# Performance work log

Measured on AMD Instinct MI355X. Metric: run time of the kernel, lower is better.

## Reference

```python
import jax, jax.numpy as jnp
import numpy as np

T, B, F_, H, D, C = 16, 1024, 512, 128, 8, 100  # trees, batch, feat, hidden, depth, classes
L = 2 ** (D + 1)  # n_leaf = 512


def _routing_tables():
    # Static per-leaf routing: node index and branch side at each depth.
    # Derived from compute_mu's gather indices:
    #   node(d, l) = 2^d - 1 + l // 2^(D+1-d);  side(d, l) = (l // 2^(D-d)) % 2
    l = np.arange(L)
    node = np.stack([(2 ** d - 1) + l // (2 ** (D + 1 - d)) for d in range(D + 1)])  # [D+1, L]
    side = np.stack([(l // (2 ** (D - d))) % 2 for d in range(D + 1)])               # [D+1, L]
    return jnp.asarray(node, dtype=jnp.int32), jnp.asarray(side.astype(np.bool_))


def setup_inputs() -> dict:
    key = jax.random.key(0)
    ks = jax.random.split(key, 4)
    return {
        "feat": jax.random.normal(ks[0], (B, F_), jnp.float32),
        "W1": jax.random.normal(ks[1], (T, F_, H), jnp.float32) * 0.05,
        "b1": jnp.zeros((T, H), jnp.float32),
        "W2": jax.random.normal(ks[2], (T, H, L), jnp.float32) * 0.05,
        "b2": jnp.zeros((T, L), jnp.float32),
        "pi": jax.random.uniform(ks[3], (T, L, C), jnp.float32, -2.0, 2.0),
    }


def reference(feat, W1, b1, W2, b2, pi):
    node, side = _routing_tables()
    # Per-tree MLP head (dropout is identity in eval mode).
    h = jax.nn.relu(jnp.einsum('bf,tfh->tbh', feat, W1) + b1[:, None, :])        # [T,B,H]
    p = jax.nn.sigmoid(jnp.einsum('tbh,thl->tbl', h, W2) + b2[:, None, :])       # [T,B,L]
    # compute_mu: product of routing probs along each root->leaf path.
    sel = p[:, :, node]                          # [T,B,D+1,L] gather (static indices)
    route = jnp.where(side, 1.0 - sel, sel)      # left -> p, right -> 1-p
    mu = jnp.prod(route, axis=2)                 # [T,B,L]
    # compute_py_x: mean over leaves then mean over trees of mu @ softmax(pi).
    leaf_p = jax.nn.softmax(pi, axis=-1)         # [T,L,C]
    py_x = jnp.einsum('tbl,tlc->bc', mu, leaf_p) / (L * T)  # [B,C]
    return jnp.log(py_x)
```

## Files before the change

### kernel.cpp

```cpp
#include <hip/hip_runtime.h>
#include <hip/hip_bf16.h>
#include <math.h>

#define T_ 16
#define B_ 1024
#define F_ 512
#define H_ 128
#define D_ 8
#define C_ 100
#define L_ 512
#define CP_ 112

typedef __attribute__((ext_vector_type(8))) short bf16x8_t;
typedef __attribute__((ext_vector_type(4))) float f32x4_t;

__device__ inline ushort f2bf(float x) {
  __hip_bfloat16 b = __float2bfloat16(x);
  return *(ushort*)&b;
}
__device__ inline float bf2f(ushort u) {
  union { unsigned int i; float f; } v;
  v.i = ((unsigned int)u) << 16;
  return v.f;
}

__device__ inline void bar_raw() {
  asm volatile("" ::: "memory");
  __builtin_amdgcn_s_barrier();
  asm volatile("" ::: "memory");
}
__device__ inline void bar_publish_lds() {
  asm volatile("s_waitcnt lgkmcnt(0)" ::: "memory");
  __builtin_amdgcn_s_barrier();
  asm volatile("" ::: "memory");
}

__global__ __launch_bounds__(256) void k_prep(
    const float* __restrict__ W1, const float* __restrict__ W2,
    const float* __restrict__ pi, ushort* __restrict__ W1T,
    ushort* __restrict__ W2T, ushort* __restrict__ lpT) {
  __shared__ float tile[64][68];
  ushort (*tileT)[48] = (ushort(*)[48])tile;
  const int bid = blockIdx.x, tid = threadIdx.x;

  if (bid < 512) {
    const float* X; ushort* XT; int K, N, kb, nb, s;
    if (bid < 256) {
      int u = bid & 15;  kb = u & 7;  nb = (u >> 3) & 1;  s = bid >> 4;
      X = W1; XT = W1T; K = F_; N = H_;
    } else {
      int r = bid - 256; int u = r & 15; kb = u & 1; nb = (u >> 1) & 7; s = r >> 4;
      X = W2; XT = W2T; K = H_; N = L_;
    }
    const int k0 = kb * 64, n0 = nb * 64;
    const float* Xs = X + (size_t)s * K * N;
    ushort* XTs = XT + (size_t)s * N * K;
    {
      const int rrow = tid >> 4, c4 = (tid & 15) * 4;
#pragma unroll
      for (int j = 0; j < 4; ++j) {
        float4 v = *(const float4*)(Xs + (size_t)(k0 + j * 16 + rrow) * N + n0 + c4);
        *(float4*)&tile[j * 16 + rrow][c4] = v;
      }
    }
    __syncthreads();
    {
      const int k8 = (tid & 7) * 8;
#pragma unroll
      for (int pass = 0; pass < 2; ++pass) {
        int rr = pass * 32 + (tid >> 3);
        bf16x8_t o;
#pragma unroll
        for (int i = 0; i < 8; ++i) o[i] = (short)f2bf(tile[k8 + i][rr]);
        *(bf16x8_t*)(XTs + (size_t)(n0 + rr) * K + k0 + k8) = o;
      }
    }
    return;
  }
  {
    int bid2 = bid - 512;
    int t = bid2 >> 4, l0 = (bid2 & 15) << 5;
    int lane = tid & 63;
#pragma unroll
    for (int p = 0; p < 8; ++p) {
      int rl = p * 4 + (tid >> 6);
      const float* x = pi + (size_t)(t * L_ + l0 + rl) * C_;
      float v0 = (lane < C_) ? x[lane] : -1e30f;
      float v1 = (lane + 64 < C_) ? x[lane + 64] : -1e30f;
      float m = fmaxf(v0, v1);
#pragma unroll
      for (int off = 32; off; off >>= 1) m = fmaxf(m, __shfl_xor(m, off, 64));
      float e0 = __expf(v0 - m);
      float e1 = (lane + 64 < C_) ? __expf(v1 - m) : 0.0f;
      float sm = e0 + e1;
#pragma unroll
      for (int off = 32; off; off >>= 1) sm += __shfl_xor(sm, off, 64);
      float inv = 1.0f / sm;
      if (lane < C_) tileT[lane][rl] = f2bf(e0 * inv);
      int c2 = lane + 64;
      if (c2 < CP_) tileT[c2][rl] = f2bf(c2 < C_ ? e1 * inv : 0.0f);
    }
    __syncthreads();
    ushort* dst = lpT + (size_t)t * CP_ * L_ + l0;
    for (int idx = tid; idx < 448; idx += 256) {
      int c = idx >> 2, ch = (idx & 3) * 8;
      *(bf16x8_t*)(dst + (size_t)c * L_ + ch) = *(const bf16x8_t*)&tileT[c][ch];
    }
  }
}

__global__ __launch_bounds__(512, 4) void k12_mfma(
    const float* __restrict__ feat, const ushort* __restrict__ W1T,
    const float* __restrict__ b1, const ushort* __restrict__ W2T,
    const float* __restrict__ b2, const ushort* __restrict__ lpT,
    float* __restrict__ part) {
  __shared__ ushort smem[38400];
  ushort (*h_s)[136] = (ushort(*)[136])smem;
  ushort (*a_s0)[72] = (ushort(*)[72])(smem + 4352);
  ushort (*a_s1)[72] = (ushort(*)[72])(smem + 4352 + 2304);
  ushort (*b_s0)[72] = (ushort(*)[72])(smem + 8960);
  ushort (*b_s1)[72] = (ushort(*)[72])(smem + 8960 + 9216);
  ushort (*w_s0)[136] = (ushort(*)[136])(smem + 4352);
  ushort (*w_s1)[136] = (ushort(*)[136])(smem + 4352 + 8704);
  ushort (*p_s)[520] = (ushort(*)[520])(smem + 21760);

  const int bid = blockIdx.x;
  const int t = bid & 15, b0 = (bid >> 4) * 32;
  const int tid = threadIdx.x;
  const int w = tid >> 6, lane = tid & 63, quad = lane >> 4, n = lane & 15;

  {
    const bool doA = tid < 256;
    const int srow = tid >> 3, scol = (tid & 7) * 8;
    const float*  fp32p = feat + (size_t)(b0 + srow) * F_ + scol;
    const ushort* w1p   = W1T + ((size_t)t * H_ + srow) * F_ + scol;

    float4 ra[2][2];
    bf16x8_t rb[2][2];

    if (doA) { ra[0][0] = *(const float4*)(fp32p);
               ra[0][1] = *(const float4*)(fp32p + 4); }
#pragma unroll
    for (int i = 0; i < 2; ++i)
      rb[0][i] = *(const bf16x8_t*)(w1p + (size_t)i * 64 * F_);
    if (doA) {
      bf16x8_t o;
      o[0] = (short)f2bf(ra[0][0].x); o[1] = (short)f2bf(ra[0][0].y);
      o[2] = (short)f2bf(ra[0][0].z); o[3] = (short)f2bf(ra[0][0].w);
      o[4] = (short)f2bf(ra[0][1].x); o[5] = (short)f2bf(ra[0][1].y);
      o[6] = (short)f2bf(ra[0][1].z); o[7] = (short)f2bf(ra[0][1].w);
      *(bf16x8_t*)&a_s0[srow][scol] = o;
    }
#pragma unroll
    for (int i = 0; i < 2; ++i)
      *(bf16x8_t*)&b_s0[i * 64 + srow][scol] = rb[0][i];
    bar_publish_lds();
    if (doA) { ra[1][0] = *(const float4*)(fp32p + 64);
               ra[1][1] = *(const float4*)(fp32p + 68); }
#pragma unroll
    for (int i = 0; i < 2; ++i)
      rb[1][i] = *(const bf16x8_t*)(w1p + (size_t)i * 64 * F_ + 64);
    if (doA) { ra[0][0] = *(const float4*)(fp32p + 128);
               ra[0][1] = *(const float4*)(fp32p + 132); }
#pragma unroll
    for (int i = 0; i < 2; ++i)
      rb[0][i] = *(const bf16x8_t*)(w1p + (size_t)i * 64 * F_ + 128);

    f32x4_t acc[2];
    acc[0] = (f32x4_t){0.f, 0.f, 0.f, 0.f};
    acc[1] = (f32x4_t){0.f, 0.f, 0.f, 0.f};
#pragma unroll
    for (int kc = 0; kc < 8; ++kc) {
      ushort (*ar)[72] = (kc & 1) ? a_s1 : a_s0;
      ushort (*br)[72] = (kc & 1) ? b_s1 : b_s0;
#pragma unroll
      for (int ks2 = 0; ks2 < 2; ++ks2) {
        const int ko = ks2 * 32 + quad * 8;
        bf16x8_t af0 = *(const bf16x8_t*)&ar[n][ko];
        bf16x8_t af1 = *(const bf16x8_t*)&ar[16 + n][ko];
        bf16x8_t bfr = *(const bf16x8_t*)&br[w * 16 + n][ko];
        acc[0] = __builtin_amdgcn_mfma_f32_16x16x32_bf16(af0, bfr, acc[0],
                                                         0, 0, 0);
        acc[1] = __builtin_amdgcn_mfma_f32_16x16x32_bf16(af1, bfr, acc[1],
                                                         0, 0, 0);
      }
      if (kc < 7) {
        const int p = (kc + 1) & 1;
        ushort (*aw)[72] = p ? a_s1 : a_s0;
        ushort (*bw)[72] = p ? b_s1 : b_s0;
        if (doA) {
          bf16x8_t o;
          o[0] = (short)f2bf(ra[p][0].x); o[1] = (short)f2bf(ra[p][0].y);
          o[2] = (short)f2bf(ra[p][0].z); o[3] = (short)f2bf(ra[p][0].w);
          o[4] = (short)f2bf(ra[p][1].x); o[5] = (short)f2bf(ra[p][1].y);
          o[6] = (short)f2bf(ra[p][1].z); o[7] = (short)f2bf(ra[p][1].w);
          *(bf16x8_t*)&aw[srow][scol] = o;
        }
#pragma unroll
        for (int i = 0; i < 2; ++i)
          *(bf16x8_t*)&bw[i * 64 + srow][scol] = rb[p][i];
        bar_publish_lds();
        if (kc < 6) {
          if (doA) { ra[p][0] = *(const float4*)(fp32p + (kc + 3) * 64);
                     ra[p][1] = *(const float4*)(fp32p + (kc + 3) * 64 + 4); }
#pragma unroll
          for (int i = 0; i < 2; ++i)
            rb[p][i] = *(const bf16x8_t*)(w1p + (size_t)i * 64 * F_ + (kc + 3) * 64);
        }
      }
    }
    float bias = b1[t * H_ + w * 16 + n];
#pragma unroll
    for (int mt = 0; mt < 2; ++mt)
#pragma unroll
      for (int r = 0; r < 4; ++r) {
        float v = acc[mt][r] + bias;
        h_s[mt * 16 + quad * 4 + r][w * 16 + n] = f2bf(v > 0.f ? v : 0.f);
      }
  }

  {
    const int wrow = tid >> 4, wcol = (tid & 15) * 8;
    const ushort* w2p = W2T + ((size_t)t * L_ + wrow) * H_ + wcol;
    bf16x8_t rw[2][2];
#pragma unroll
    for (int i = 0; i < 2; ++i)
      rw[0][i] = *(const bf16x8_t*)(w2p + (size_t)(i * 32) * H_);
#pragma unroll
    for (int i = 0; i < 2; ++i)
      rw[1][i] = *(const bf16x8_t*)(w2p + (size_t)(64 + i * 32) * H_);
    bar_publish_lds();

    const int mhalf = w >> 2, lhalf = w & 3;
    bf16x8_t af2[4];
#pragma unroll
    for (int ks = 0; ks < 4; ++ks)
      af2[ks] = *(const bf16x8_t*)&h_s[mhalf * 16 + n][ks * 32 + quad * 8];
#pragma unroll
    for (int i = 0; i < 2; ++i)
      *(bf16x8_t*)&w_s0[i * 32 + wrow][wcol] = rw[0][i];
    bar_publish_lds();
#pragma unroll
    for (int i = 0; i < 2; ++i)
      rw[0][i] = *(const bf16x8_t*)(w2p + (size_t)(128 + i * 32) * H_);

#pragma unroll
    for (int nc = 0; nc < 8; ++nc) {
      ushort (*wr)[136] = (nc & 1) ? w_s1 : w_s0;
      f32x4_t acc = (f32x4_t){0.f, 0.f, 0.f, 0.f};
#pragma unroll
      for (int ks = 0; ks < 4; ++ks) {
        bf16x8_t bfrag = *(const bf16x8_t*)&wr[lhalf * 16 + n][ks * 32 + quad * 8];
        acc = __builtin_amdgcn_mfma_f32_16x16x32_bf16(af2[ks], bfrag, acc,
                                                      0, 0, 0);
      }
      int l = nc * 64 + lhalf * 16 + n;
      float bias = b2[t * L_ + l];
#pragma unroll
      for (int r = 0; r < 4; ++r) {
        float x = acc[r] + bias;
        p_s[mhalf * 16 + quad * 4 + r][l] = f2bf(1.0f / (1.0f + __expf(-x)));
      }
      if (nc < 7) {
        const int p = (nc + 1) & 1;
        ushort (*ww)[136] = p ? w_s1 : w_s0;
#pragma unroll
        for (int i = 0; i < 2; ++i)
          *(bf16x8_t*)&ww[i * 32 + wrow][wcol] = rw[p][i];
        bar_publish_lds();
        if (nc < 6) {
#pragma unroll
          for (int i = 0; i < 2; ++i)
            rw[p][i] = *(const bf16x8_t*)(w2p + (size_t)((nc + 3) * 64 + i * 32) * H_);
        }
      }
    }
  }
  bar_publish_lds();

  bf16x8_t mo[2][2];
#pragma unroll
  for (int pass = 0; pass < 2; ++pass) {
    int unit = pass * 512 + tid;
    int b = unit >> 5;
    int s = unit & 31;
    float P = 1.f;
#pragma unroll
    for (int d = 0; d < 5; ++d) {
      int nd = (1 << d) - 1 + (s >> (5 - d));
      int sd = (s >> (4 - d)) & 1;
      float pv = bf2f(p_s[b][nd]);
      P *= sd ? (1.f - pv) : pv;
    }
    float p5 = bf2f(p_s[b][31 + s]);
    float q5[2] = {P * p5, P * (1.f - p5)};
    float q6[4], q7[8];
#pragma unroll
    for (int j = 0; j < 2; ++j) {
      float pv = bf2f(p_s[b][63 + 2 * s + j]);
      q6[2 * j] = q5[j] * pv;
      q6[2 * j + 1] = q5[j] * (1.f - pv);
    }
#pragma unroll
    for (int u = 0; u < 4; ++u) {
      float pv = bf2f(p_s[b][127 + 4 * s + u]);
      q7[2 * u] = q6[u] * pv;
      q7[2 * u + 1] = q6[u] * (1.f - pv);
    }
    bf16x8_t o0, o1;
#pragma unroll
    for (int v = 0; v < 8; ++v) {
      float pv = bf2f(p_s[b][255 + 8 * s + v]);
      ushort e0 = f2bf(q7[v] * pv);
      ushort e1 = f2bf(q7[v] * (1.f - pv));
      if (v < 4) { o0[2 * v] = (short)e0; o0[2 * v + 1] = (short)e1; }
      else       { o1[2 * (v - 4)] = (short)e0; o1[2 * (v - 4) + 1] = (short)e1; }
    }
    mo[pass][0] = o0;
    mo[pass][1] = o1;
  }
  bar_raw();
#pragma unroll
  for (int pass = 0; pass < 2; ++pass) {
    int unit = pass * 512 + tid;
    int b = unit >> 5;
    int s = unit & 31;
    *(bf16x8_t*)&p_s[b][s * 16]     = mo[pass][0];
    *(bf16x8_t*)&p_s[b][s * 16 + 8] = mo[pass][1];
  }
  bar_publish_lds();

  {
#pragma unroll
    for (int uu = 0; uu < 2; ++uu) {
      int u = w + uu * 8;
      if (u < 14) {
        const int mt = u & 1, nt = u >> 1;
        const ushort* arow = &p_s[mt * 16 + n][0];
        const ushort* brow = lpT + (size_t)t * CP_ * L_ +
                             ((size_t)(nt * 16 + n)) * L_ + quad * 8;
        f32x4_t acc = (f32x4_t){0.f, 0.f, 0.f, 0.f};
#pragma unroll 4
        for (int k = 0; k < L_; k += 32) {
          bf16x8_t af = *(const bf16x8_t*)(arow + k + quad * 8);
          bf16x8_t bfr = *(const bf16x8_t*)(brow + k);
          acc = __builtin_amdgcn_mfma_f32_16x16x32_bf16(af, bfr, acc, 0, 0, 0);
        }
        const int m0 = b0 + mt * 16 + quad * 4;
        const int c = nt * 16 + n;
        if (c < C_) {
#pragma unroll
          for (int r = 0; r < 4; ++r)
            part[((size_t)t * B_ + m0 + r) * C_ + c] = acc[r];
        }
      }
    }
  }
}

__global__ __launch_bounds__(256) void k6_log(
    const float* __restrict__ part, float* __restrict__ out) {
  int i = (blockIdx.x * 256 + threadIdx.x) * 4;
  if (i < B_ * C_) {
    float4 s = {0.f, 0.f, 0.f, 0.f};
#pragma unroll
    for (int t = 0; t < T_; ++t) {
      float4 v = *(const float4*)(part + (size_t)t * B_ * C_ + i);
      s.x += v.x; s.y += v.y; s.z += v.z; s.w += v.w;
    }
    const float inv = 1.0f / (L_ * T_);
    float4 o;
    o.x = logf(s.x * inv); o.y = logf(s.y * inv);
    o.z = logf(s.z * inv); o.w = logf(s.w * inv);
    *(float4*)(out + i) = o;
  }
}

extern "C" void kernel_launch(void* const* d_in, const int* in_sizes, int n_in,
                              void* d_out, int out_size, void* d_ws,
                              size_t ws_size, hipStream_t stream) {
  const float* feat = (const float*)d_in[0];
  const float* W1   = (const float*)d_in[1];
  const float* b1   = (const float*)d_in[2];
  const float* W2   = (const float*)d_in[3];
  const float* b2   = (const float*)d_in[4];
  const float* pi   = (const float*)d_in[5];
  float* out = (float*)d_out;

  char* ws = (char*)d_ws;
  ushort* W1T_buf  = (ushort*)(ws);
  ushort* W2T_buf  = (ushort*)(ws + ((size_t)2 << 20));
  ushort* lpT_buf  = (ushort*)(ws + ((size_t)4 << 20));
  float*  part_buf = (float*)(ws + ((size_t)6 << 20));

  k_prep<<<768, 256, 0, stream>>>(W1, W2, pi, W1T_buf, W2T_buf, lpT_buf);
  k12_mfma<<<512, 512, 0, stream>>>(feat, W1T_buf, b1, W2T_buf, b2,
                                    lpT_buf, part_buf);
  k6_log<<<(B_ * C_ / 4 + 255) / 256, 256, 0, stream>>>(part_buf, out);
}
```

Before: 108.3 us.

## Double per-block batch tile to 64 rows to halve weight reloads

Each block now processes 64 batch rows instead of 32, halving the grid to 256 blocks. Every block still loads the full per-tree W1, W2 and leaf-distribution weights, so total weight traffic from global memory drops by half. Shared memory grows to about 136KB and the launch bound drops to 2 blocks per CU. With 256 blocks on a 256-CU part, each CU gets a single block and latency hiding may suffer. An extra barrier was added before the double-buffer writes.

```diff
diff --git a/kernel.cpp b/kernel.cpp
--- a/kernel.cpp
+++ b/kernel.cpp
@@ -109,28 +109,27 @@
   }
 }
 
-__global__ __launch_bounds__(512, 4) void k12_mfma(
+__global__ __launch_bounds__(512, 2) void k12_mfma(
     const float* __restrict__ feat, const ushort* __restrict__ W1T,
     const float* __restrict__ b1, const ushort* __restrict__ W2T,
     const float* __restrict__ b2, const ushort* __restrict__ lpT,
     float* __restrict__ part) {
-  __shared__ ushort smem[38400];
+  __shared__ ushort smem[69632];
   ushort (*h_s)[136] = (ushort(*)[136])smem;
-  ushort (*a_s0)[72] = (ushort(*)[72])(smem + 4352);
-  ushort (*a_s1)[72] = (ushort(*)[72])(smem + 4352 + 2304);
-  ushort (*b_s0)[72] = (ushort(*)[72])(smem + 8960);
-  ushort (*b_s1)[72] = (ushort(*)[72])(smem + 8960 + 9216);
-  ushort (*w_s0)[136] = (ushort(*)[136])(smem + 4352);
-  ushort (*w_s1)[136] = (ushort(*)[136])(smem + 4352 + 8704);
-  ushort (*p_s)[520] = (ushort(*)[520])(smem + 21760);
+  ushort (*a_s0)[72] = (ushort(*)[72])(smem + 8704);
+  ushort (*a_s1)[72] = (ushort(*)[72])(smem + 8704 + 4608);
+  ushort (*b_s0)[72] = (ushort(*)[72])(smem + 17920);
+  ushort (*b_s1)[72] = (ushort(*)[72])(smem + 17920 + 9216);
+  ushort (*w_s0)[136] = (ushort(*)[136])(smem + 8704);
+  ushort (*w_s1)[136] = (ushort(*)[136])(smem + 8704 + 8704);
+  ushort (*p_s)[520] = (ushort(*)[520])(smem + 36352);
 
   const int bid = blockIdx.x;
-  const int t = bid & 15, b0 = (bid >> 4) * 32;
+  const int t = bid & 15, b0 = (bid >> 4) * 64;
   const int tid = threadIdx.x;
   const int w = tid >> 6, lane = tid & 63, quad = lane >> 4, n = lane & 15;
 
   {
-    const bool doA = tid < 256;
     const int srow = tid >> 3, scol = (tid & 7) * 8;
     const float*  fp32p = feat + (size_t)(b0 + srow) * F_ + scol;
     const ushort* w1p   = W1T + ((size_t)t * H_ + srow) * F_ + scol;
@@ -138,12 +137,12 @@
     float4 ra[2][2];
     bf16x8_t rb[2][2];
 
-    if (doA) { ra[0][0] = *(const float4*)(fp32p);
-               ra[0][1] = *(const float4*)(fp32p + 4); }
+    ra[0][0] = *(const float4*)(fp32p);
+    ra[0][1] = *(const float4*)(fp32p + 4);
 #pragma unroll
     for (int i = 0; i < 2; ++i)
       rb[0][i] = *(const bf16x8_t*)(w1p + (size_t)i * 64 * F_);
-    if (doA) {
+    {
       bf16x8_t o;
       o[0] = (short)f2bf(ra[0][0].x); o[1] = (short)f2bf(ra[0][0].y);
       o[2] = (short)f2bf(ra[0][0].z); o[3] = (short)f2bf(ra[0][0].w);
@@ -155,20 +154,20 @@
     for (int i = 0; i < 2; ++i)
       *(bf16x8_t*)&b_s0[i * 64 + srow][scol] = rb[0][i];
     bar_publish_lds();
-    if (doA) { ra[1][0] = *(const float4*)(fp32p + 64);
-               ra[1][1] = *(const float4*)(fp32p + 68); }
+    ra[1][0] = *(const float4*)(fp32p + 64);
+    ra[1][1] = *(const float4*)(fp32p + 68);
 #pragma unroll
     for (int i = 0; i < 2; ++i)
       rb[1][i] = *(const bf16x8_t*)(w1p + (size_t)i * 64 * F_ + 64);
-    if (doA) { ra[0][0] = *(const float4*)(fp32p + 128);
-               ra[0][1] = *(const float4*)(fp32p + 132); }
+    ra[0][0] = *(const float4*)(fp32p + 128);
+    ra[0][1] = *(const float4*)(fp32p + 132);
 #pragma unroll
     for (int i = 0; i < 2; ++i)
       rb[0][i] = *(const bf16x8_t*)(w1p + (size_t)i * 64 * F_ + 128);
 
-    f32x4_t acc[2];
-    acc[0] = (f32x4_t){0.f, 0.f, 0.f, 0.f};
-    acc[1] = (f32x4_t){0.f, 0.f, 0.f, 0.f};
+    f32x4_t acc[4];
+#pragma unroll
+    for (int i = 0; i < 4; ++i) acc[i] = (f32x4_t){0.f, 0.f, 0.f, 0.f};
 #pragma unroll
     for (int kc = 0; kc < 8; ++kc) {
       ushort (*ar)[72] = (kc & 1) ? a_s1 : a_s0;
@@ -176,19 +175,20 @@
 #pragma unroll
       for (int ks2 = 0; ks2 < 2; ++ks2) {
         const int ko = ks2 * 32 + quad * 8;
-        bf16x8_t af0 = *(const bf16x8_t*)&ar[n][ko];
-        bf16x8_t af1 = *(const bf16x8_t*)&ar[16 + n][ko];
         bf16x8_t bfr = *(const bf16x8_t*)&br[w * 16 + n][ko];
-        acc[0] = __builtin_amdgcn_mfma_f32_16x16x32_bf16(af0, bfr, acc[0],
-                                                         0, 0, 0);
-        acc[1] = __builtin_amdgcn_mfma_f32_16x16x32_bf16(af1, bfr, acc[1],
-                                                         0, 0, 0);
+#pragma unroll
+        for (int mt = 0; mt < 4; ++mt) {
+          bf16x8_t af = *(const bf16x8_t*)&ar[mt * 16 + n][ko];
+          acc[mt] = __builtin_amdgcn_mfma_f32_16x16x32_bf16(af, bfr, acc[mt],
+                                                            0, 0, 0);
+        }
       }
       if (kc < 7) {
         const int p = (kc + 1) & 1;
         ushort (*aw)[72] = p ? a_s1 : a_s0;
         ushort (*bw)[72] = p ? b_s1 : b_s0;
-        if (doA) {
+        bar_raw();
+        {
           bf16x8_t o;
           o[0] = (short)f2bf(ra[p][0].x); o[1] = (short)f2bf(ra[p][0].y);
           o[2] = (short)f2bf(ra[p][0].z); o[3] = (short)f2bf(ra[p][0].w);
@@ -201,8 +201,8 @@
           *(bf16x8_t*)&bw[i * 64 + srow][scol] = rb[p][i];
         bar_publish_lds();
         if (kc < 6) {
-          if (doA) { ra[p][0] = *(const float4*)(fp32p + (kc + 3) * 64);
-                     ra[p][1] = *(const float4*)(fp32p + (kc + 3) * 64 + 4); }
+          ra[p][0] = *(const float4*)(fp32p + (kc + 3) * 64);
+          ra[p][1] = *(const float4*)(fp32p + (kc + 3) * 64 + 4);
 #pragma unroll
           for (int i = 0; i < 2; ++i)
             rb[p][i] = *(const bf16x8_t*)(w1p + (size_t)i * 64 * F_ + (kc + 3) * 64);
@@ -211,7 +211,7 @@
     }
     float bias = b1[t * H_ + w * 16 + n];
 #pragma unroll
-    for (int mt = 0; mt < 2; ++mt)
+    for (int mt = 0; mt < 4; ++mt)
 #pragma unroll
       for (int r = 0; r < 4; ++r) {
         float v = acc[mt][r] + bias;
@@ -231,11 +231,11 @@
       rw[1][i] = *(const bf16x8_t*)(w2p + (size_t)(64 + i * 32) * H_);
     bar_publish_lds();
 
-    const int mhalf = w >> 2, lhalf = w & 3;
+    const int mt2 = w >> 1, lh = w & 1;
     bf16x8_t af2[4];
 #pragma unroll
     for (int ks = 0; ks < 4; ++ks)
-      af2[ks] = *(const bf16x8_t*)&h_s[mhalf * 16 + n][ks * 32 + quad * 8];
+      af2[ks] = *(const bf16x8_t*)&h_s[mt2 * 16 + n][ks * 32 + quad * 8];
 #pragma unroll
     for (int i = 0; i < 2; ++i)
       *(bf16x8_t*)&w_s0[i * 32 + wrow][wcol] = rw[0][i];
@@ -247,19 +247,27 @@
 #pragma unroll
     for (int nc = 0; nc < 8; ++nc) {
       ushort (*wr)[136] = (nc & 1) ? w_s1 : w_s0;
-      f32x4_t acc = (f32x4_t){0.f, 0.f, 0.f, 0.f};
-#pragma unroll
-      for (int ks = 0; ks < 4; ++ks) {
-        bf16x8_t bfrag = *(const bf16x8_t*)&wr[lhalf * 16 + n][ks * 32 + quad * 8];
-        acc = __builtin_amdgcn_mfma_f32_16x16x32_bf16(af2[ks], bfrag, acc,
-                                                      0, 0, 0);
-      }
-      int l = nc * 64 + lhalf * 16 + n;
-      float bias = b2[t * L_ + l];
-#pragma unroll
-      for (int r = 0; r < 4; ++r) {
-        float x = acc[r] + bias;
-        p_s[mhalf * 16 + quad * 4 + r][l] = f2bf(1.0f / (1.0f + __expf(-x)));
+      f32x4_t acc2[2];
+      acc2[0] = (f32x4_t){0.f, 0.f, 0.f, 0.f};
+      acc2[1] = (f32x4_t){0.f, 0.f, 0.f, 0.f};
+#pragma unroll
+      for (int lt = 0; lt < 2; ++lt)
+#pragma unroll
+        for (int ks = 0; ks < 4; ++ks) {
+          bf16x8_t bfrag =
+              *(const bf16x8_t*)&wr[lh * 32 + lt * 16 + n][ks * 32 + quad * 8];
+          acc2[lt] = __builtin_amdgcn_mfma_f32_16x16x32_bf16(af2[ks], bfrag,
+                                                             acc2[lt], 0, 0, 0);
+        }
+#pragma unroll
+      for (int lt = 0; lt < 2; ++lt) {
+        int l = nc * 64 + lh * 32 + lt * 16 + n;
+        float bias = b2[t * L_ + l];
+#pragma unroll
+        for (int r = 0; r < 4; ++r) {
+          float x = acc2[lt][r] + bias;
+          p_s[mt2 * 16 + quad * 4 + r][l] = f2bf(1.0f / (1.0f + __expf(-x)));
+        }
       }
       if (nc < 7) {
         const int p = (nc + 1) & 1;
@@ -278,9 +286,9 @@
   }
   bar_publish_lds();
 
-  bf16x8_t mo[2][2];
-#pragma unroll
-  for (int pass = 0; pass < 2; ++pass) {
+  bf16x8_t mo[4][2];
+#pragma unroll
+  for (int pass = 0; pass < 4; ++pass) {
     int unit = pass * 512 + tid;
     int b = unit >> 5;
     int s = unit & 31;
@@ -321,7 +329,7 @@
   }
   bar_raw();
 #pragma unroll
-  for (int pass = 0; pass < 2; ++pass) {
+  for (int pass = 0; pass < 4; ++pass) {
     int unit = pass * 512 + tid;
     int b = unit >> 5;
     int s = unit & 31;
@@ -332,10 +340,10 @@
 
   {
 #pragma unroll
-    for (int uu = 0; uu < 2; ++uu) {
+    for (int uu = 0; uu < 4; ++uu) {
       int u = w + uu * 8;
-      if (u < 14) {
-        const int mt = u & 1, nt = u >> 1;
+      if (u < 28) {
+        const int mt = u & 3, nt = u >> 2;
         const ushort* arow = &p_s[mt * 16 + n][0];
         const ushort* brow = lpT + (size_t)t * CP_ * L_ +
                              ((size_t)(nt * 16 + n)) * L_ + quad * 8;
@@ -394,7 +402,7 @@
   float*  part_buf = (float*)(ws + ((size_t)6 << 20));
 
   k_prep<<<768, 256, 0, stream>>>(W1, W2, pi, W1T_buf, W2T_buf, lpT_buf);
-  k12_mfma<<<512, 512, 0, stream>>>(feat, W1T_buf, b1, W2T_buf, b2,
+  k12_mfma<<<256, 512, 0, stream>>>(feat, W1T_buf, b1, W2T_buf, b2,
                                     lpT_buf, part_buf);
   k6_log<<<(B_ * C_ / 4 + 255) / 256, 256, 0, stream>>>(part_buf, out);
 }
```

Result: slower. 111.6 us (+3.1%).
